# Kernel optimization log

Measured on AMD Instinct MI355X. Metric: run time of the kernel, lower is better.

The kernel has to match this reference:

```python
import jax, jax.numpy as jnp
import numpy as np

ALPHA = 0.2  # LeakyReLU negative slope


def setup_inputs() -> dict:
    key = jax.random.key(0)
    k1, k2, k3, k4 = jax.random.split(key, 4)
    N, E, d_in, d_out = 100000, 1600000, 64, 64
    node_features = jax.random.normal(k1, (N, d_in), dtype=jnp.float32)
    edge_index = jax.random.randint(k2, (2, E), 0, N, dtype=jnp.int64)
    # learned params: W is Linear(in,out,bias=False) weight used as x @ W.T; store as [d_in,d_out]
    W = jax.random.normal(k3, (d_in, d_out), dtype=jnp.float32) * (1.414 * np.sqrt(2.0 / (d_in + d_out)))
    a = jax.random.normal(k4, (2 * d_out,), dtype=jnp.float32) * (1.414 * np.sqrt(2.0 / (2 * d_out + 1)))
    return {"node_features": node_features, "edge_index": edge_index, "W": W, "a": a}


def reference(node_features, edge_index, W, a):
    N = node_features.shape[0]
    d_out = W.shape[1]
    src, tgt = edge_index[0], edge_index[1]

    h = node_features @ W  # [N, d_out]
    # a([h_src, h_tgt]) == h_src @ a[:d] + h_tgt @ a[d:]; compute node-level scores once
    s_src = h @ a[:d_out]   # [N]
    s_tgt = h @ a[d_out:]   # [N]
    e = jax.nn.leaky_relu(s_src[src] + s_tgt[tgt], negative_slope=ALPHA)  # [E]

    # per-target segment softmax (stable): scatter-max, exp, scatter-sum
    m = jax.ops.segment_max(e, tgt, num_segments=N)          # [N]
    e_exp = jnp.exp(e - m[tgt])                              # [E]
    denom = jax.ops.segment_sum(e_exp, tgt, num_segments=N)  # [N]
    attention = e_exp / denom[tgt]                           # [E]
    # dropout is identity in eval mode (training=False)

    # weighted scatter-add of source features into targets
    h_prime = jax.ops.segment_sum(h[src] * attention[:, None], tgt, num_segments=N)  # [N, d_out]
    return jax.nn.elu(h_prime)
```

## Files before the change

kernel.cpp:

```cpp
#include <hip/hip_runtime.h>
#include <hip/hip_bf16.h>
#include <math.h>

#define ALPHA  0.2f
#define BSH    6
#define BNODES 64
#define NBMAX  1600
#define K_CH   4096
#define CAPB   2048
#define SCH    7

static __device__ __forceinline__ unsigned short f2bf(float x) {
    __hip_bfloat16 b = __float2bfloat16(x);
    return *reinterpret_cast<unsigned short*>(&b);
}

__global__ __launch_bounds__(256) void k_prep(
    const float* __restrict__ X, const float* __restrict__ W,
    const float* __restrict__ a, unsigned short* __restrict__ hb,
    float* __restrict__ s_src, float* __restrict__ s_tgt,
    const int* __restrict__ src, const int* __restrict__ tgt,
    int* __restrict__ cur, int* __restrict__ ebuf,
    int N, int E, int nb, int gFill)
{
    __shared__ __align__(16) char smem[37632];
    const int tid = threadIdx.x;

    if (blockIdx.x >= gFill) {
        float (*Xs)[65] = (float(*)[65])smem;
        float (*Ws)[64] = (float(*)[64])(smem + 16640);
        const int row0 = (blockIdx.x - gFill) * 64;

        {
            const float4* W4 = (const float4*)W;
            float4* Wd = (float4*)&Ws[0][0];
            for (int q = tid; q < 1024; q += 256) Wd[q] = W4[q];
        }
        for (int q = tid; q < 1024; q += 256) {
            int r  = q >> 4;
            int c4 = (q & 15) * 4;
            int row = row0 + r;
            float4 v = make_float4(0.f, 0.f, 0.f, 0.f);
            if (row < N) v = *(const float4*)&X[(size_t)row * 64 + c4];
            Xs[r][c4 + 0] = v.x; Xs[r][c4 + 1] = v.y;
            Xs[r][c4 + 2] = v.z; Xs[r][c4 + 3] = v.w;
        }
        __syncthreads();

        const int cg = (tid & 15) * 4;
        const int rg = (tid >> 4) * 4;

        float acc[4][4];
#pragma unroll
        for (int r = 0; r < 4; ++r)
#pragma unroll
            for (int c = 0; c < 4; ++c) acc[r][c] = 0.f;

#pragma unroll 8
        for (int k = 0; k < 64; ++k) {
            float4 wv = *(const float4*)&Ws[k][cg];
            float x0 = Xs[rg + 0][k], x1 = Xs[rg + 1][k];
            float x2 = Xs[rg + 2][k], x3 = Xs[rg + 3][k];
            acc[0][0] += x0 * wv.x; acc[0][1] += x0 * wv.y; acc[0][2] += x0 * wv.z; acc[0][3] += x0 * wv.w;
            acc[1][0] += x1 * wv.x; acc[1][1] += x1 * wv.y; acc[1][2] += x1 * wv.z; acc[1][3] += x1 * wv.w;
            acc[2][0] += x2 * wv.x; acc[2][1] += x2 * wv.y; acc[2][2] += x2 * wv.z; acc[2][3] += x2 * wv.w;
            acc[3][0] += x3 * wv.x; acc[3][1] += x3 * wv.y; acc[3][2] += x3 * wv.z; acc[3][3] += x3 * wv.w;
        }

        float a1[4], a2[4];
#pragma unroll
        for (int c = 0; c < 4; ++c) { a1[c] = a[cg + c]; a2[c] = a[64 + cg + c]; }

#pragma unroll
        for (int r = 0; r < 4; ++r) {
            int row = row0 + rg + r;
            if (row < N) {
                ushort4 hv;
                hv.x = f2bf(acc[r][0]); hv.y = f2bf(acc[r][1]);
                hv.z = f2bf(acc[r][2]); hv.w = f2bf(acc[r][3]);
                *(ushort4*)&hb[(size_t)row * 64 + cg] = hv;
            }
            float v1 = acc[r][0]*a1[0] + acc[r][1]*a1[1] + acc[r][2]*a1[2] + acc[r][3]*a1[3];
            float v2 = acc[r][0]*a2[0] + acc[r][1]*a2[1] + acc[r][2]*a2[2] + acc[r][3]*a2[3];
            v1 += __shfl_xor(v1, 1); v2 += __shfl_xor(v2, 1);
            v1 += __shfl_xor(v1, 2); v2 += __shfl_xor(v2, 2);
            v1 += __shfl_xor(v1, 4); v2 += __shfl_xor(v2, 4);
            v1 += __shfl_xor(v1, 8); v2 += __shfl_xor(v2, 8);
            if ((tid & 15) == 0 && row < N) { s_src[row] = v1; s_tgt[row] = v2; }
        }
    } else {
        int* pk    = (int*)smem;
        int* hist  = (int*)(smem + 16384);
        int* off_s = (int*)(smem + 22784);
        int* gbase = (int*)(smem + 29184);
        int* part  = (int*)(smem + 35584);

        const int blk = blockIdx.x;
        const int e0  = blk * K_CH;
        const int e1  = min(e0 + K_CH, E);
        const int cnt = e1 - e0;

        for (int i = tid; i < nb; i += 256) hist[i] = 0;
        __syncthreads();

        for (int i = e0 + tid; i < e1; i += 256)
            atomicAdd(&hist[tgt[i] >> BSH], 1);
        __syncthreads();

        int pref[SCH];
        {
            int s = 0;
            const int i0 = tid * SCH;
#pragma unroll
            for (int j = 0; j < SCH; ++j) {
                int idx = i0 + j;
                int v = (idx < nb) ? hist[idx] : 0;
                pref[j] = s;
                s += v;
            }
            part[tid] = s;
        }
        __syncthreads();
#pragma unroll
        for (int o = 1; o < 256; o <<= 1) {
            int t2 = (tid >= o) ? part[tid - o] : 0;
            __syncthreads();
            part[tid] += t2;
            __syncthreads();
        }
        {
            const int base0 = (tid > 0) ? part[tid - 1] : 0;
            const int i0 = tid * SCH;
#pragma unroll
            for (int j = 0; j < SCH; ++j) {
                int idx = i0 + j;
                if (idx < nb) off_s[idx] = base0 + pref[j];
            }
        }
        __syncthreads();

        for (int i = tid; i < nb; i += 256) {
            int c = hist[i];
            if (c) {
                int within = atomicAdd(&cur[i], c);
                gbase[i] = i * CAPB + within;
            }
            hist[i] = off_s[i];
        }
        __syncthreads();

        for (int i = e0 + tid; i < e1; i += 256) {
            int t = tgt[i];
            int b = t >> BSH;
            int p = atomicAdd(&hist[b], 1);
            pk[p] = src[i] | ((t & (BNODES - 1)) << 17);
        }
        __syncthreads();

        for (int i = tid; i < cnt; i += 256) {
            int lo = 0, hi = nb;
            while (hi - lo > 1) {
                int mid = (lo + hi) >> 1;
                if (off_s[mid] <= i) lo = mid; else hi = mid;
            }
            int rel = i - off_s[lo];
            int gb  = gbase[lo];
            if ((gb & (CAPB - 1)) + rel < CAPB) ebuf[gb + rel] = pk[i];
        }
    }
}

__global__ __launch_bounds__(256) void k_bgather(
    const int* __restrict__ cur, const int* __restrict__ ebuf,
    const float* __restrict__ s_src, const float* __restrict__ s_tgt,
    const uint2* __restrict__ hb2,
    float* __restrict__ out, int N)
{
    __shared__ int   ssrc[CAPB];
    __shared__ float sexp[CAPB];
    __shared__ int   hist[BNODES];
    __shared__ int   off_s[BNODES + 1];
    __shared__ int   cur_s[BNODES];
    __shared__ float sT[BNODES];

    const int tid  = threadIdx.x;
    const int b    = blockIdx.x;
    const int base = b << BSH;
    const int nn   = min(BNODES, N - base);
    const int beg  = b * CAPB;
    const int cnt  = min(cur[b], CAPB);

    if (tid < BNODES) {
        hist[tid] = 0;
        sT[tid] = (base + tid < N) ? s_tgt[base + tid] : 0.f;
    }
    __syncthreads();

    for (int i = tid; i < cnt; i += 256)
        atomicAdd(&hist[(ebuf[beg + i] >> 17) & (BNODES - 1)], 1);
    __syncthreads();

    if (tid < 64) {
        int v = hist[tid];
        int incl = v;
#pragma unroll
        for (int o = 1; o < 64; o <<= 1) {
            int t2 = __shfl_up(incl, o);
            if (tid >= o) incl += t2;
        }
        off_s[tid + 1] = incl;
        cur_s[tid]     = incl - v;
        if (tid == 0) off_s[0] = 0;
    }
    __syncthreads();

    for (int i = tid; i < cnt; i += 256) {
        int pkv  = ebuf[beg + i];
        int toff = (pkv >> 17) & (BNODES - 1);
        int sv   = pkv & 0x1FFFF;
        int pos  = atomicAdd(&cur_s[toff], 1);
        float sc = s_src[sv] + sT[toff];
        sc = (sc >= 0.f) ? sc : ALPHA * sc;
        ssrc[pos] = sv;
        sexp[pos] = __expf(sc);
    }
    __syncthreads();

    const int w     = tid >> 6;
    const int lane  = tid & 63;
    const int g     = lane >> 4;
    const int fidx2 = lane & 15;

    for (int tl = w; tl < nn; tl += 4) {
        const int t    = base + tl;
        const int beg2 = off_s[tl];
        const int c    = off_s[tl + 1] - beg2;
        const unsigned ocol = (unsigned)t * 64 + fidx2 * 4;

        if (c == 0) {
            if (g == 0) *(float4*)&out[ocol] = make_float4(0.f, 0.f, 0.f, 0.f);
            continue;
        }

        float ax = 0.f, ay = 0.f, az = 0.f, aw = 0.f, den = 0.f;
        for (int k = 0; k < c; k += 4) {
            int idx = k + g;
            int cl  = beg2 + min(idx, c - 1);
            int sv  = ssrc[cl];
            float pe = (idx < c) ? sexp[cl] : 0.f;
            uint2 u = hb2[((unsigned)sv << 4) + fidx2];
            den += pe;
            ax += pe * __uint_as_float(u.x << 16);
            ay += pe * __uint_as_float(u.x & 0xFFFF0000u);
            az += pe * __uint_as_float(u.y << 16);
            aw += pe * __uint_as_float(u.y & 0xFFFF0000u);
        }
        ax += __shfl_xor(ax, 16); ay += __shfl_xor(ay, 16);
        az += __shfl_xor(az, 16); aw += __shfl_xor(aw, 16);
        den += __shfl_xor(den, 16);
        ax += __shfl_xor(ax, 32); ay += __shfl_xor(ay, 32);
        az += __shfl_xor(az, 32); aw += __shfl_xor(aw, 32);
        den += __shfl_xor(den, 32);

        if (g == 0) {
            float rd = 1.f / den;
            float r0 = ax * rd, r1 = ay * rd, r2 = az * rd, r3 = aw * rd;
            r0 = (r0 > 0.f) ? r0 : expm1f(r0);
            r1 = (r1 > 0.f) ? r1 : expm1f(r1);
            r2 = (r2 > 0.f) ? r2 : expm1f(r2);
            r3 = (r3 > 0.f) ? r3 : expm1f(r3);
            *(float4*)&out[ocol] = make_float4(r0, r1, r2, r3);
        }
    }
}

extern "C" void kernel_launch(void* const* d_in, const int* in_sizes, int n_in,
                              void* d_out, int out_size, void* d_ws, size_t ws_size,
                              hipStream_t stream)
{
    const float* X  = (const float*)d_in[0];
    const int*   ei = (const int*)d_in[1];
    const float* W  = (const float*)d_in[2];
    const float* a  = (const float*)d_in[3];

    const int N = in_sizes[0] / 64;
    const int E = in_sizes[1] / 2;
    const int* src = ei;
    const int* tgt = ei + E;

    float* out = (float*)d_out;

    const int nb    = (N + BNODES - 1) >> BSH;
    const int nbA   = (N + 63) / 64;
    const int gFill = (E + K_CH - 1) / K_CH;

    char* ws = (char*)d_ws;
    unsigned short* hb = (unsigned short*)ws; ws += (size_t)N * 64 * sizeof(unsigned short);
    float* s_src  = (float*)ws; ws += (size_t)N * sizeof(float);
    float* s_tgt  = (float*)ws; ws += (size_t)N * sizeof(float);
    int*   cur    = (int*)ws;   ws += (size_t)nb * sizeof(int);
    int*   ebuf   = (int*)ws;   ws += (size_t)nb * CAPB * sizeof(int);

    hipMemsetAsync(cur, 0, (size_t)nb * sizeof(int), stream);

    k_prep    <<<gFill + nbA, 256, 0, stream>>>(X, W, a, hb, s_src, s_tgt,
                                                src, tgt, cur, ebuf, N, E, nb, gFill);
    k_bgather <<<nb, 256, 0, stream>>>(cur, ebuf, s_src, s_tgt,
                                       (const uint2*)hb, out, N);
}
```

Measured before the change: 109.7 us.

## Scatter edges directly to global buckets and transpose X tile in prep

The bucketing path no longer stages packed edges in shared memory and then runs a binary search over bucket offsets to copy them out. Each edge is now written straight to its global bucket slot, using the atomic position and the per-bucket base. This frees shared memory, which allows a larger edge chunk per block (fewer fill blocks) and trims the LDS footprint. The GEMM tile of X is stored transposed so each thread reads its four row values with one vector LDS load, at the cost of a strided transposed store. The direct global writes are less coalesced than the old bucket-contiguous copy, and the larger chunk halves the number of fill blocks available for parallelism.

Result: slower. 116.7 us (+6.5%).

```diff
diff --git a/kernel.cpp b/kernel.cpp
--- a/kernel.cpp
+++ b/kernel.cpp
@@ -6,7 +6,7 @@
 #define BSH    6
 #define BNODES 64
 #define NBMAX  1600
-#define K_CH   4096
+#define K_CH   8192
 #define CAPB   2048
 #define SCH    7
 
@@ -23,12 +23,12 @@
     int* __restrict__ cur, int* __restrict__ ebuf,
     int N, int E, int nb, int gFill)
 {
-    __shared__ __align__(16) char smem[37632];
+    __shared__ __align__(16) char smem[33792];
     const int tid = threadIdx.x;
 
     if (blockIdx.x >= gFill) {
-        float (*Xs)[65] = (float(*)[65])smem;
-        float (*Ws)[64] = (float(*)[64])(smem + 16640);
+        float (*XsT)[65] = (float(*)[65])smem;
+        float (*Ws)[64]  = (float(*)[64])(smem + 16640);
         const int row0 = (blockIdx.x - gFill) * 64;
 
         {
@@ -42,8 +42,8 @@
             int row = row0 + r;
             float4 v = make_float4(0.f, 0.f, 0.f, 0.f);
             if (row < N) v = *(const float4*)&X[(size_t)row * 64 + c4];
-            Xs[r][c4 + 0] = v.x; Xs[r][c4 + 1] = v.y;
-            Xs[r][c4 + 2] = v.z; Xs[r][c4 + 3] = v.w;
+            XsT[c4 + 0][r] = v.x; XsT[c4 + 1][r] = v.y;
+            XsT[c4 + 2][r] = v.z; XsT[c4 + 3][r] = v.w;
         }
         __syncthreads();
 
@@ -59,12 +59,11 @@
 #pragma unroll 8
         for (int k = 0; k < 64; ++k) {
             float4 wv = *(const float4*)&Ws[k][cg];
-            float x0 = Xs[rg + 0][k], x1 = Xs[rg + 1][k];
-            float x2 = Xs[rg + 2][k], x3 = Xs[rg + 3][k];
-            acc[0][0] += x0 * wv.x; acc[0][1] += x0 * wv.y; acc[0][2] += x0 * wv.z; acc[0][3] += x0 * wv.w;
-            acc[1][0] += x1 * wv.x; acc[1][1] += x1 * wv.y; acc[1][2] += x1 * wv.z; acc[1][3] += x1 * wv.w;
-            acc[2][0] += x2 * wv.x; acc[2][1] += x2 * wv.y; acc[2][2] += x2 * wv.z; acc[2][3] += x2 * wv.w;
-            acc[3][0] += x3 * wv.x; acc[3][1] += x3 * wv.y; acc[3][2] += x3 * wv.z; acc[3][3] += x3 * wv.w;
+            float4 xv = *(const float4*)&XsT[k][rg];
+            acc[0][0] += xv.x * wv.x; acc[0][1] += xv.x * wv.y; acc[0][2] += xv.x * wv.z; acc[0][3] += xv.x * wv.w;
+            acc[1][0] += xv.y * wv.x; acc[1][1] += xv.y * wv.y; acc[1][2] += xv.y * wv.z; acc[1][3] += xv.y * wv.w;
+            acc[2][0] += xv.z * wv.x; acc[2][1] += xv.z * wv.y; acc[2][2] += xv.z * wv.z; acc[2][3] += xv.z * wv.w;
+            acc[3][0] += xv.w * wv.x; acc[3][1] += xv.w * wv.y; acc[3][2] += xv.w * wv.z; acc[3][3] += xv.w * wv.w;
         }
 
         float a1[4], a2[4];
@@ -89,16 +88,14 @@
             if ((tid & 15) == 0 && row < N) { s_src[row] = v1; s_tgt[row] = v2; }
         }
     } else {
-        int* pk    = (int*)smem;
-        int* hist  = (int*)(smem + 16384);
-        int* off_s = (int*)(smem + 22784);
-        int* gbase = (int*)(smem + 29184);
-        int* part  = (int*)(smem + 35584);
+        int* hist  = (int*)smem;
+        int* off_s = (int*)(smem + 6400);
+        int* gbase = (int*)(smem + 12800);
+        int* part  = (int*)(smem + 19200);
 
         const int blk = blockIdx.x;
         const int e0  = blk * K_CH;
         const int e1  = min(e0 + K_CH, E);
-        const int cnt = e1 - e0;
 
         for (int i = tid; i < nb; i += 256) hist[i] = 0;
         __syncthreads();
@@ -153,19 +150,10 @@
             int t = tgt[i];
             int b = t >> BSH;
             int p = atomicAdd(&hist[b], 1);
-            pk[p] = src[i] | ((t & (BNODES - 1)) << 17);
-        }
-        __syncthreads();
-
-        for (int i = tid; i < cnt; i += 256) {
-            int lo = 0, hi = nb;
-            while (hi - lo > 1) {
-                int mid = (lo + hi) >> 1;
-                if (off_s[mid] <= i) lo = mid; else hi = mid;
-            }
-            int rel = i - off_s[lo];
-            int gb  = gbase[lo];
-            if ((gb & (CAPB - 1)) + rel < CAPB) ebuf[gb + rel] = pk[i];
+            int rel = p - off_s[b];
+            int gb  = gbase[b];
+            if ((gb & (CAPB - 1)) + rel < CAPB)
+                ebuf[gb + rel] = src[i] | ((t & (BNODES - 1)) << 17);
         }
     }
 }
```
